# Kernel optimization log

Hardware: AMD Instinct MI355X
Metric: run time of the kernel (lower is better)

## Reference

```python
import jax, jax.numpy as jnp
import numpy as np

EPS = 1e-5

def _make_mask(rng, outdim, indim, expand_size, k=3):
    # Mirrors ExpanderConv2d mask construction (indim <= outdim branch when equal)
    m = np.zeros((outdim, indim), dtype=np.float32)
    if indim > outdim:
        for i in range(outdim):
            idx = rng.permutation(indim)[:expand_size]
            m[i, idx] = 1.0
    else:
        for i in range(indim):
            idx = rng.permutation(outdim)[:expand_size]
            m[idx, i] = 1.0
    return jnp.asarray(np.broadcast_to(m[:, :, None, None], (outdim, indim, k, k)).copy())

def _bn(x, gamma, beta, mean, var):
    # eval-mode BatchNorm2d over channel axis (NCHW)
    inv = gamma / jnp.sqrt(var + EPS)
    return x * inv[None, :, None, None] + (beta - mean * inv)[None, :, None, None]

def _conv3x3(x, w, stride=1):
    return jax.lax.conv_general_dilated(
        x, w, window_strides=(stride, stride), padding=((1, 1), (1, 1)),
        dimension_numbers=('NCHW', 'OIHW', 'NCHW'))

def setup_inputs() -> dict:
    key = jax.random.key(0)
    ks = jax.random.split(key, 4)
    C = 256
    x = jax.random.normal(ks[0], (64, C, 32, 32), dtype=jnp.float32)
    fan_out = C * 9
    std = float(np.sqrt(2.0 / fan_out))  # kaiming_normal_, mode='fan_out'
    w1 = jax.random.normal(ks[1], (C, C, 3, 3), dtype=jnp.float32) * std
    w2 = jax.random.normal(ks[2], (C, C, 3, 3), dtype=jnp.float32) * std
    rng = np.random.default_rng(0)
    mask1 = _make_mask(rng, C, C, C // 8)
    mask2 = _make_mask(rng, C, C, C // 8)
    g = jax.random.uniform(ks[3], (4 * C,), minval=0.5, maxval=1.5, dtype=jnp.float32)
    return {
        'x': x,
        'bn1_gamma': g[:C], 'bn1_beta': jnp.zeros((C,), jnp.float32),
        'bn1_mean': jnp.zeros((C,), jnp.float32), 'bn1_var': jnp.ones((C,), jnp.float32),
        'w1': w1, 'mask1': mask1,
        'bn2_gamma': g[C:2 * C], 'bn2_beta': jnp.zeros((C,), jnp.float32),
        'bn2_mean': jnp.zeros((C,), jnp.float32), 'bn2_var': jnp.ones((C,), jnp.float32),
        'w2': w2, 'mask2': mask2,
    }

def reference(x, bn1_gamma, bn1_beta, bn1_mean, bn1_var, w1, mask1,
              bn2_gamma, bn2_beta, bn2_mean, bn2_var, w2, mask2):
    out = jax.nn.relu(_bn(x, bn1_gamma, bn1_beta, bn1_mean, bn1_var))
    out = _conv3x3(out, w1 * mask1)          # masked expander conv, dropout(p=0)=identity
    out = jax.nn.relu(_bn(out, bn2_gamma, bn2_beta, bn2_mean, bn2_var))
    out = _conv3x3(out, w2 * mask2, stride=1)
    return out + x                            # identity shortcut (stride=1, in==out)
```

## Files before the change

### kernel.cpp

```cpp
#include <hip/hip_runtime.h>
#include <hip/hip_bf16.h>
#include <stdint.h>

typedef __bf16 bf16_t;
typedef __bf16 bf16x8 __attribute__((ext_vector_type(8)));
typedef __bf16 bf16x4 __attribute__((ext_vector_type(4)));
typedef float  f32x4  __attribute__((ext_vector_type(4)));

#define AS_GLOBAL __attribute__((address_space(1)))
#define AS_LDS    __attribute__((address_space(3)))

static constexpr int CCH   = 256;
static constexpr int HP    = 34;
static constexpr int PLANE = HP * HP;

__global__ void prep_params_k(const float* g1, const float* b1, const float* m1, const float* v1,
                              const float* g2, const float* b2, const float* m2, const float* v2,
                              float* prm) {
  int i = threadIdx.x;
  float i1 = g1[i] * rsqrtf(v1[i] + 1e-5f);
  prm[i]       = i1;
  prm[256 + i] = b1[i] - m1[i] * i1;
  float i2 = g2[i] * rsqrtf(v2[i] + 1e-5f);
  prm[512 + i] = i2;
  prm[768 + i] = b2[i] - m2[i] * i2;
}

__global__ __launch_bounds__(256) void prep_weights_k(const float* __restrict__ w,
                                                      const float* __restrict__ msk,
                                                      bf16_t* __restrict__ out) {
  int idx = blockIdx.x * 256 + threadIdx.x;
  const float* wp = w + (long)idx * 9;
  const float* mp = msk + (long)idx * 9;
#pragma unroll
  for (int khw = 0; khw < 9; ++khw)
    out[khw * 65536 + idx] = (bf16_t)(wp[khw] * mp[khw]);
}

__global__ __launch_bounds__(256) void zero_borders_k(bf16_t* __restrict__ t0p,
                                                      bf16_t* __restrict__ t1p) {
  const int bid = blockIdx.x;
  bf16_t* base = ((bid & 1) ? t1p : t0p) + (long)(bid >> 1) * PLANE * CCH;
  for (int i = threadIdx.x; i < 132 * 32; i += 256) {
    int pix = i >> 5, c16 = i & 31;
    int r, col;
    if (pix < 34)       { r = 0;           col = pix; }
    else if (pix < 68)  { r = 33;          col = pix - 34; }
    else if (pix < 100) { r = pix - 68 + 1; col = 0; }
    else                { r = pix - 100 + 1; col = 33; }
    *(f32x4*)&base[(r * HP + col) * CCH + c16 * 8] = f32x4{0.f, 0.f, 0.f, 0.f};
  }
}

__global__ __launch_bounds__(256) void prep_input_k(const float* __restrict__ x,
                                                    const float* __restrict__ prm,
                                                    bf16_t* __restrict__ t0p) {
  __shared__ __align__(16) bf16_t tile[64 * 256];
  const int tid = threadIdx.x;
  const int bid = blockIdx.x;
  const int n   = bid >> 4;
  const int p0  = (bid & 15) << 6;
  const int px    = tid & 63;
  const int cbase = tid >> 6;
  for (int r = 0; r < 64; ++r) {
    int ci = r * 4 + cbase;
    float v = x[((n * 256 + ci) << 10) + p0 + px];
    float y = fmaxf(v * prm[ci] + prm[256 + ci], 0.f);
    int byte = px * 512 + ((ci * 2) ^ ((px & 7) << 4));
    *(bf16_t*)((char*)tile + byte) = (bf16_t)y;
  }
  __syncthreads();
  for (int j = 0; j < 8; ++j) {
    int off  = j * 256 + tid;
    int pix  = off >> 5;
    int c16  = off & 31;
    int byte = pix * 512 + ((c16 * 16) ^ ((pix & 7) << 4));
    bf16x8 v = *(const bf16x8*)((char*)tile + byte);
    int p = p0 + pix;
    long gp = ((long)n * PLANE + ((p >> 5) + 1) * HP + (p & 31) + 1) * CCH + c16 * 8;
    *(bf16x8*)(t0p + gp) = v;
  }
}

template <int EPI>
__global__ __launch_bounds__(256, 2) void conv3x3_k(const bf16_t* __restrict__ inp,
                                                    const bf16_t* __restrict__ wts,
                                                    const float* __restrict__ prm,
                                                    const float* __restrict__ resid,
                                                    bf16_t* __restrict__ out_cl,
                                                    float* __restrict__ out_f) {
  __shared__ __align__(128) bf16_t As[2][4096];
  __shared__ __align__(128) bf16_t Bs[2][8192];

  const int tid  = threadIdx.x;
  const int lane = tid & 63;
  const int wid  = tid >> 6;
  const int wm   = wid >> 1;
  const int wn   = wid & 1;

  const int bid = blockIdx.x;
  const int w   = ((bid & 7) << 7) + (bid >> 3);
  const int co0 = (w & 1) << 7;
  const int pt  = w >> 1;
  const int n   = pt >> 3;
  const int hb  = (pt & 7) << 2;

  const int swz8 = (((lane & 3) ^ ((lane >> 2) & 3) ^ (lane >> 4)) << 3);
  const int l15  = lane & 15;

  f32x4 acc[4][4];
#pragma unroll
  for (int i = 0; i < 4; ++i)
#pragma unroll
    for (int j = 0; j < 4; ++j) acc[i][j] = f32x4{0.f, 0.f, 0.f, 0.f};

  auto stageA = [&](int ab, int c, int t) {
    const int ci0 = c << 5;
#pragma unroll
    for (int j = 0; j < 2; ++j) {
      const int ch  = wid * 2 + j;
      const int row = ch * 16 + (lane >> 2);
      const bf16_t* ga = wts + ((t * CCH + co0 + row) * CCH + ci0 + swz8);
      __builtin_amdgcn_global_load_lds((const AS_GLOBAL void*)ga,
                                       (AS_LDS void*)(&As[ab][ch * 512]), 16, 0, 0);
    }
  };

  auto stageB = [&](int bb, int c) {
    const int ci0 = c << 5;
#pragma unroll
    for (int j = 0; j < 4; ++j) {
      const int ibase = wid * 4 + j;
      int g = (ibase << 6) + lane;
      if (g > 815) g = 815;
      const int r  = g / 136;
      const int rm = g - r * 136;
      const bf16_t* gb = inp + ((n * PLANE + (hb + r) * HP + (rm >> 2)) * CCH + ci0 + ((rm & 3) << 3));
      __builtin_amdgcn_global_load_lds((const AS_GLOBAL void*)gb,
                                       (AS_LDS void*)(&Bs[bb][ibase * 512]), 16, 0, 0);
    }
  };

  stageB(0, 0);
  stageA(0, 0, 0);
  int ab = 0, bb = 0;
  for (int c = 0; c < 8; ++c) {
#pragma unroll
    for (int t = 0; t < 9; ++t) {
      __syncthreads();
      if (t < 8) stageA(ab ^ 1, c, t + 1);
      else if (c < 7) { stageB(bb ^ 1, c + 1); stageA(ab ^ 1, c + 1, 0); }
      const int kh = t / 3, kw = t - kh * 3;
      bf16x8 av[4], bv[4];
#pragma unroll
      for (int mi = 0; mi < 4; ++mi)
        av[mi] = *(const bf16x8*)&As[ab][((wm * 64 + mi * 16 + l15) << 5) + swz8];
#pragma unroll
      for (int ni = 0; ni < 4; ++ni) {
        const int p  = (wn << 6) + (ni << 4) + l15;
        const int pr = p >> 5, pc = p & 31;
        bv[ni] = *(const bf16x8*)&Bs[bb][((pr + kh) * 136 + (pc + kw) * 4 + (lane >> 4)) * 8];
      }
#pragma unroll
      for (int mi = 0; mi < 4; ++mi)
#pragma unroll
        for (int ni = 0; ni < 4; ++ni)
          acc[mi][ni] = __builtin_amdgcn_mfma_f32_16x16x32_bf16(av[mi], bv[ni], acc[mi][ni], 0, 0, 0);
      ab ^= 1;
    }
    bb ^= 1;
  }

  if (EPI == 0) {
#pragma unroll
    for (int mi = 0; mi < 4; ++mi) {
      const int co_b = co0 + wm * 64 + mi * 16 + ((lane >> 4) << 2);
      const float s0 = prm[co_b], s1 = prm[co_b + 1], s2 = prm[co_b + 2], s3 = prm[co_b + 3];
      const float t0 = prm[256 + co_b], t1 = prm[256 + co_b + 1],
                  t2 = prm[256 + co_b + 2], t3 = prm[256 + co_b + 3];
#pragma unroll
      for (int ni = 0; ni < 4; ++ni) {
        f32x4 v = acc[mi][ni];
        const int p  = (wn << 6) + (ni << 4) + l15;
        const int pr = p >> 5, pc = p & 31;
        bf16x4 pk;
        pk[0] = (bf16_t)fmaxf(v[0] * s0 + t0, 0.f);
        pk[1] = (bf16_t)fmaxf(v[1] * s1 + t1, 0.f);
        pk[2] = (bf16_t)fmaxf(v[2] * s2 + t2, 0.f);
        pk[3] = (bf16_t)fmaxf(v[3] * s3 + t3, 0.f);
        *(bf16x4*)&out_cl[(n * PLANE + (hb + pr + 1) * HP + pc + 1) * CCH + co_b] = pk;
      }
    }
  } else {
#pragma unroll
    for (int mi = 0; mi < 4; ++mi) {
      const int co_b = co0 + wm * 64 + mi * 16 + ((lane >> 4) << 2);
#pragma unroll
      for (int ni = 0; ni < 4; ++ni) {
        f32x4 v = acc[mi][ni];
        const int p  = (wn << 6) + (ni << 4) + l15;
        const int gp = ((n * CCH + co_b) << 10) + (hb << 5) + p;
        out_f[gp]        = v[0] + resid[gp];
        out_f[gp + 1024] = v[1] + resid[gp + 1024];
        out_f[gp + 2048] = v[2] + resid[gp + 2048];
        out_f[gp + 3072] = v[3] + resid[gp + 3072];
      }
    }
  }
}

extern "C" void kernel_launch(void* const* d_in, const int* in_sizes, int n_in,
                              void* d_out, int out_size, void* d_ws, size_t ws_size,
                              hipStream_t stream) {
  const float* x  = (const float*)d_in[0];
  const float* g1 = (const float*)d_in[1];
  const float* b1 = (const float*)d_in[2];
  const float* m1 = (const float*)d_in[3];
  const float* v1 = (const float*)d_in[4];
  const float* w1 = (const float*)d_in[5];
  const float* k1 = (const float*)d_in[6];
  const float* g2 = (const float*)d_in[7];
  const float* b2 = (const float*)d_in[8];
  const float* m2 = (const float*)d_in[9];
  const float* v2 = (const float*)d_in[10];
  const float* w2 = (const float*)d_in[11];
  const float* k2 = (const float*)d_in[12];

  char* ws = (char*)d_ws;
  const size_t T0P_B = (size_t)64 * PLANE * CCH * 2;
  bf16_t* t0p = (bf16_t*)ws;
  bf16_t* t1p = (bf16_t*)(ws + T0P_B);
  bf16_t* mw1 = (bf16_t*)(ws + 2 * T0P_B);
  bf16_t* mw2 = (bf16_t*)(ws + 2 * T0P_B + 1179648);
  float*  prm = (float*)(ws + 2 * T0P_B + 2 * 1179648);

  prep_params_k<<<1, 256, 0, stream>>>(g1, b1, m1, v1, g2, b2, m2, v2, prm);
  zero_borders_k<<<128, 256, 0, stream>>>(t0p, t1p);
  prep_weights_k<<<256, 256, 0, stream>>>(w1, k1, mw1);
  prep_weights_k<<<256, 256, 0, stream>>>(w2, k2, mw2);
  prep_input_k<<<1024, 256, 0, stream>>>(x, prm, t0p);

  conv3x3_k<0><<<1024, 256, 0, stream>>>(t0p, mw1, prm + 512, nullptr, t1p, nullptr);
  conv3x3_k<1><<<1024, 256, 0, stream>>>(t1p, mw2, nullptr, x, nullptr, (float*)d_out);
}
```

Before: 200.6 us.

## Deepen weight prefetch to five LDS buffers with explicit vmcnt waits

Turns the double-buffered weight (A) staging into a 5-deep ring that runs four taps ahead. It replaces __syncthreads with partial s_waitcnt vmcnt plus s_barrier, so async global-to-LDS loads stay in flight across iterations. It also rotates the B-tile channel-chunk placement to cut LDS bank conflicts on the shifted-window reads, and peels the last channel chunk into its own loop. LDS per block grows from 48KB to 72KB, which may cut occupancy below the two blocks per CU requested by launch_bounds. The hand-counted vmcnt values are fragile.

Result: no change. 203.3 us (+1.3%).

```diff
diff --git a/kernel.cpp b/kernel.cpp
--- a/kernel.cpp
+++ b/kernel.cpp
@@ -9,6 +9,7 @@
 
 #define AS_GLOBAL __attribute__((address_space(1)))
 #define AS_LDS    __attribute__((address_space(3)))
+#define VMW(N) asm volatile("s_waitcnt vmcnt(" #N ")" ::: "memory")
 
 static constexpr int CCH   = 256;
 static constexpr int HP    = 34;
@@ -89,7 +90,7 @@
                                                     const float* __restrict__ resid,
                                                     bf16_t* __restrict__ out_cl,
                                                     float* __restrict__ out_f) {
-  __shared__ __align__(128) bf16_t As[2][4096];
+  __shared__ __align__(128) bf16_t As[5][4096];
   __shared__ __align__(128) bf16_t Bs[2][8192];
 
   const int tid  = threadIdx.x;
@@ -107,6 +108,7 @@
 
   const int swz8 = (((lane & 3) ^ ((lane >> 2) & 3) ^ (lane >> 4)) << 3);
   const int l15  = lane & 15;
+  const int k4   = lane >> 4;
 
   f32x4 acc[4][4];
 #pragma unroll
@@ -114,7 +116,7 @@
 #pragma unroll
     for (int j = 0; j < 4; ++j) acc[i][j] = f32x4{0.f, 0.f, 0.f, 0.f};
 
-  auto stageA = [&](int ab, int c, int t) {
+  auto stageA = [&](int abuf, int c, int t) {
     const int ci0 = c << 5;
 #pragma unroll
     for (int j = 0; j < 2; ++j) {
@@ -122,53 +124,73 @@
       const int row = ch * 16 + (lane >> 2);
       const bf16_t* ga = wts + ((t * CCH + co0 + row) * CCH + ci0 + swz8);
       __builtin_amdgcn_global_load_lds((const AS_GLOBAL void*)ga,
-                                       (AS_LDS void*)(&As[ab][ch * 512]), 16, 0, 0);
+                                       (AS_LDS void*)(&As[abuf][ch * 512]), 16, 0, 0);
     }
   };
 
-  auto stageB = [&](int bb, int c) {
+  auto stageB = [&](int bbuf, int c) {
     const int ci0 = c << 5;
 #pragma unroll
     for (int j = 0; j < 4; ++j) {
       const int ibase = wid * 4 + j;
-      int g = (ibase << 6) + lane;
-      if (g > 815) g = 815;
-      const int r  = g / 136;
-      const int rm = g - r * 136;
-      const bf16_t* gb = inp + ((n * PLANE + (hb + r) * HP + (rm >> 2)) * CCH + ci0 + ((rm & 3) << 3));
+      int s = (ibase << 6) + lane;
+      if (s > 815) s = 815;
+      const int r     = s / 136;
+      const int rem   = s - r * 136;
+      const int cc    = rem >> 2;
+      const int k     = ((rem & 3) - (cc >> 1)) & 3;
+      const bf16_t* gb = inp + ((n * PLANE + (hb + r) * HP + cc) * CCH + ci0 + (k << 3));
       __builtin_amdgcn_global_load_lds((const AS_GLOBAL void*)gb,
-                                       (AS_LDS void*)(&Bs[bb][ibase * 512]), 16, 0, 0);
+                                       (AS_LDS void*)(&Bs[bbuf][ibase * 512]), 16, 0, 0);
     }
   };
 
+  auto compute = [&](int abuf, int bbuf, int kh, int kw) {
+    bf16x8 av[4], bv[4];
+#pragma unroll
+    for (int mi = 0; mi < 4; ++mi)
+      av[mi] = *(const bf16x8*)&As[abuf][((wm * 64 + mi * 16 + l15) << 5) + swz8];
+#pragma unroll
+    for (int ni = 0; ni < 4; ++ni) {
+      const int p    = (wn << 6) + (ni << 4) + l15;
+      const int cc   = (p & 31) + kw;
+      const int slot = ((p >> 5) + kh) * 136 + (cc << 2) + ((k4 + (cc >> 1)) & 3);
+      bv[ni] = *(const bf16x8*)&Bs[bbuf][slot << 3];
+    }
+#pragma unroll
+    for (int mi = 0; mi < 4; ++mi)
+#pragma unroll
+      for (int ni = 0; ni < 4; ++ni)
+        acc[mi][ni] = __builtin_amdgcn_mfma_f32_16x16x32_bf16(av[mi], bv[ni], acc[mi][ni], 0, 0, 0);
+  };
+
   stageB(0, 0);
-  stageA(0, 0, 0);
-  int ab = 0, bb = 0;
-  for (int c = 0; c < 8; ++c) {
+  stageA(0, 0, 0); stageA(1, 0, 1); stageA(2, 0, 2); stageA(3, 0, 3);
+
+  int ab = 0;
+  for (int c = 0; c < 7; ++c) {
 #pragma unroll
     for (int t = 0; t < 9; ++t) {
-      __syncthreads();
-      if (t < 8) stageA(ab ^ 1, c, t + 1);
-      else if (c < 7) { stageB(bb ^ 1, c + 1); stageA(ab ^ 1, c + 1, 0); }
-      const int kh = t / 3, kw = t - kh * 3;
-      bf16x8 av[4], bv[4];
-#pragma unroll
-      for (int mi = 0; mi < 4; ++mi)
-        av[mi] = *(const bf16x8*)&As[ab][((wm * 64 + mi * 16 + l15) << 5) + swz8];
-#pragma unroll
-      for (int ni = 0; ni < 4; ++ni) {
-        const int p  = (wn << 6) + (ni << 4) + l15;
-        const int pr = p >> 5, pc = p & 31;
-        bv[ni] = *(const bf16x8*)&Bs[bb][((pr + kh) * 136 + (pc + kw) * 4 + (lane >> 4)) * 8];
-      }
-#pragma unroll
-      for (int mi = 0; mi < 4; ++mi)
-#pragma unroll
-        for (int ni = 0; ni < 4; ++ni)
-          acc[mi][ni] = __builtin_amdgcn_mfma_f32_16x16x32_bf16(av[mi], bv[ni], acc[mi][ni], 0, 0, 0);
-      ab ^= 1;
-    }
-    bb ^= 1;
+      if (t >= 1 && t <= 3) { VMW(10); } else { VMW(6); }
+      __builtin_amdgcn_s_barrier();
+      if (t == 0) stageB((c + 1) & 1, c + 1);
+      int aw = ab + 4; if (aw >= 5) aw -= 5;
+      if (t < 5) stageA(aw, c, t + 4);
+      else       stageA(aw, c + 1, t - 5);
+      compute(ab, c & 1, t / 3, t % 3);
+      ++ab; if (ab == 5) ab = 0;
+    }
+  }
+#pragma unroll
+  for (int t = 0; t < 9; ++t) {
+    if      (t == 6) { VMW(4); }
+    else if (t == 7) { VMW(2); }
+    else if (t == 8) { VMW(0); }
+    else             { VMW(6); }
+    __builtin_amdgcn_s_barrier();
+    if (t < 5) { int aw = ab + 4; if (aw >= 5) aw -= 5; stageA(aw, 7, t + 4); }
+    compute(ab, 1, t / 3, t % 3);
+    ++ab; if (ab == 5) ab = 0;
   }
 
   if (EPI == 0) {
```

## Enlarge conv tile to 256x256 with 8 waves and triple-buffered weight pipeline

Applied to the files above, without the earlier changes.

Each block now computes all 256 output channels for 8 rows (256 pixels) using 512 threads, so the input halo tile is staged once per block instead of twice. Weights are triple-buffered and loaded in halves, with explicit vmcnt waits, raw barriers and setprio around the MFMA groups to overlap loads with compute. The B tile gets a rotated swizzle to reduce LDS bank conflicts. The grid shrinks to 256 blocks, which is about one block per CU on this chip and may leave little latency hiding. The larger accumulator (128 floats per lane) also adds register pressure.

Measured after the change: 193.9 us. 3.3% less time.

```diff
diff --git a/kernel.cpp b/kernel.cpp
--- a/kernel.cpp
+++ b/kernel.cpp
@@ -9,6 +9,7 @@
 
 #define AS_GLOBAL __attribute__((address_space(1)))
 #define AS_LDS    __attribute__((address_space(3)))
+#define VMW(N) asm volatile("s_waitcnt vmcnt(" #N ")" ::: "memory")
 
 static constexpr int CCH   = 256;
 static constexpr int HP    = 34;
@@ -83,98 +84,131 @@
 }
 
 template <int EPI>
-__global__ __launch_bounds__(256, 2) void conv3x3_k(const bf16_t* __restrict__ inp,
+__global__ __launch_bounds__(512, 2) void conv3x3_k(const bf16_t* __restrict__ inp,
                                                     const bf16_t* __restrict__ wts,
                                                     const float* __restrict__ prm,
                                                     const float* __restrict__ resid,
                                                     bf16_t* __restrict__ out_cl,
                                                     float* __restrict__ out_f) {
-  __shared__ __align__(128) bf16_t As[2][4096];
-  __shared__ __align__(128) bf16_t Bs[2][8192];
+  __shared__ __align__(128) bf16_t As[3][8192];
+  __shared__ __align__(128) bf16_t Bs[2][12288];
 
   const int tid  = threadIdx.x;
   const int lane = tid & 63;
   const int wid  = tid >> 6;
-  const int wm   = wid >> 1;
-  const int wn   = wid & 1;
+  const int wm   = wid >> 2;
+  const int wn   = wid & 3;
 
   const int bid = blockIdx.x;
-  const int w   = ((bid & 7) << 7) + (bid >> 3);
-  const int co0 = (w & 1) << 7;
-  const int pt  = w >> 1;
-  const int n   = pt >> 3;
-  const int hb  = (pt & 7) << 2;
+  const int n   = bid >> 2;
+  const int hb  = (bid & 3) << 3;
 
   const int swz8 = (((lane & 3) ^ ((lane >> 2) & 3) ^ (lane >> 4)) << 3);
   const int l15  = lane & 15;
-
-  f32x4 acc[4][4];
-#pragma unroll
-  for (int i = 0; i < 4; ++i)
+  const int k4   = lane >> 4;
+
+  f32x4 acc[8][4];
+#pragma unroll
+  for (int i = 0; i < 8; ++i)
 #pragma unroll
     for (int j = 0; j < 4; ++j) acc[i][j] = f32x4{0.f, 0.f, 0.f, 0.f};
 
-  auto stageA = [&](int ab, int c, int t) {
-    const int ci0 = c << 5;
-#pragma unroll
-    for (int j = 0; j < 2; ++j) {
-      const int ch  = wid * 2 + j;
-      const int row = ch * 16 + (lane >> 2);
-      const bf16_t* ga = wts + ((t * CCH + co0 + row) * CCH + ci0 + swz8);
-      __builtin_amdgcn_global_load_lds((const AS_GLOBAL void*)ga,
-                                       (AS_LDS void*)(&As[ab][ch * 512]), 16, 0, 0);
-    }
+  bf16x8 av[8], bv[4];
+
+  auto stageA_half = [&](int abuf, int c, int t, int half) {
+    const int ch  = wid * 2 + half;
+    const int row = ch * 16 + (lane >> 2);
+    const bf16_t* ga = wts + ((t * CCH + row) * CCH + (c << 5) + swz8);
+    __builtin_amdgcn_global_load_lds((const AS_GLOBAL void*)ga,
+                                     (AS_LDS void*)(&As[abuf][ch * 512]), 16, 0, 0);
   };
 
-  auto stageB = [&](int bb, int c) {
-    const int ci0 = c << 5;
-#pragma unroll
-    for (int j = 0; j < 4; ++j) {
-      const int ibase = wid * 4 + j;
-      int g = (ibase << 6) + lane;
-      if (g > 815) g = 815;
-      const int r  = g / 136;
-      const int rm = g - r * 136;
-      const bf16_t* gb = inp + ((n * PLANE + (hb + r) * HP + (rm >> 2)) * CCH + ci0 + ((rm & 3) << 3));
-      __builtin_amdgcn_global_load_lds((const AS_GLOBAL void*)gb,
-                                       (AS_LDS void*)(&Bs[bb][ibase * 512]), 16, 0, 0);
-    }
+  auto stageB = [&](int bbuf, int c, int j) {
+    const int ibase = wid * 3 + j;
+    int s = (ibase << 6) + lane;
+    if (s > 1359) s = 1359;
+    const int r   = s / 136;
+    const int rem = s - r * 136;
+    const int cc  = rem >> 2;
+    const int ks  = ((rem & 3) - (cc >> 1)) & 3;
+    const bf16_t* gb = inp + ((n * PLANE + (hb + r) * HP + cc) * CCH + (c << 5) + (ks << 3));
+    __builtin_amdgcn_global_load_lds((const AS_GLOBAL void*)gb,
+                                     (AS_LDS void*)(&Bs[bbuf][ibase * 512]), 16, 0, 0);
   };
 
-  stageB(0, 0);
-  stageA(0, 0, 0);
-  int ab = 0, bb = 0;
-  for (int c = 0; c < 8; ++c) {
-#pragma unroll
-    for (int t = 0; t < 9; ++t) {
-      __syncthreads();
-      if (t < 8) stageA(ab ^ 1, c, t + 1);
-      else if (c < 7) { stageB(bb ^ 1, c + 1); stageA(ab ^ 1, c + 1, 0); }
-      const int kh = t / 3, kw = t - kh * 3;
-      bf16x8 av[4], bv[4];
-#pragma unroll
-      for (int mi = 0; mi < 4; ++mi)
-        av[mi] = *(const bf16x8*)&As[ab][((wm * 64 + mi * 16 + l15) << 5) + swz8];
-#pragma unroll
-      for (int ni = 0; ni < 4; ++ni) {
-        const int p  = (wn << 6) + (ni << 4) + l15;
-        const int pr = p >> 5, pc = p & 31;
-        bv[ni] = *(const bf16x8*)&Bs[bb][((pr + kh) * 136 + (pc + kw) * 4 + (lane >> 4)) * 8];
-      }
-#pragma unroll
-      for (int mi = 0; mi < 4; ++mi)
-#pragma unroll
-        for (int ni = 0; ni < 4; ++ni)
-          acc[mi][ni] = __builtin_amdgcn_mfma_f32_16x16x32_bf16(av[mi], bv[ni], acc[mi][ni], 0, 0, 0);
-      ab ^= 1;
-    }
-    bb ^= 1;
-  }
+#define LDA(AB) do {                                                                \
+    _Pragma("unroll") for (int mi = 0; mi < 8; ++mi)                                \
+      av[mi] = *(const bf16x8*)&As[AB][((wm * 128 + mi * 16 + l15) << 5) + swz8];   \
+  } while (0)
+
+#define LDB(T, BB) do {                                                             \
+    constexpr int KH = (T) / 3, KW = (T) % 3;                                       \
+    _Pragma("unroll") for (int ni = 0; ni < 4; ++ni) {                              \
+      const int p_    = (wn << 6) + (ni << 4) + l15;                                \
+      const int cc_   = (p_ & 31) + KW;                                             \
+      const int slot_ = ((p_ >> 5) + KH) * 136 + (cc_ << 2) + ((k4 + (cc_ >> 1)) & 3); \
+      bv[ni] = *(const bf16x8*)&Bs[BB][slot_ << 3];                                 \
+    }                                                                               \
+  } while (0)
+
+#define MFMA8(NJ) do {                                                              \
+    _Pragma("unroll") for (int mi = 0; mi < 8; ++mi)                                \
+      acc[mi][NJ] = __builtin_amdgcn_mfma_f32_16x16x32_bf16(av[mi], bv[NJ], acc[mi][NJ], 0, 0, 0); \
+  } while (0)
+
+#define TILE(t, CL7) do {                                                           \
+    constexpr int AB  = (t) % 3;                                                    \
+    constexpr int AB2 = ((t) + 2) % 3;                                              \
+    const int bb = c & 1;                                                           \
+                                       \
+    LDA(AB); LDB(t, bb);                                                            \
+    if ((CL7) && ((t) == 1 || (t) == 3 || (t) == 5)) stageB(bb ^ 1, c + 1, ((t) - 1) / 2); \
+    if ((CL7) || (t) <= 6) {                                                        \
+      if ((t) <= 6) stageA_half(AB2, c, (t) + 2, 0);                                \
+      else          stageA_half(AB2, c + 1, (t) - 7, 0);                            \
+    }                                                                               \
+    __builtin_amdgcn_s_barrier();                                                   \
+    asm volatile("s_waitcnt lgkmcnt(0)" ::: "memory");                              \
+    __builtin_amdgcn_sched_barrier(0);                                              \
+    __builtin_amdgcn_s_setprio(1); MFMA8(0); MFMA8(1); __builtin_amdgcn_s_setprio(0); \
+    __builtin_amdgcn_s_barrier();                                                   \
+                                   \
+    if ((CL7) || (t) <= 6) {                                                        \
+      if ((t) <= 6) stageA_half(AB2, c, (t) + 2, 1);                                \
+      else          stageA_half(AB2, c + 1, (t) - 7, 1);                            \
+    }                                                                               \
+    __builtin_amdgcn_s_setprio(1); MFMA8(2); MFMA8(3); __builtin_amdgcn_s_setprio(0); \
+    if ((CL7) || (t) <= 6) {                                                        \
+      if ((CL7) && ((t) == 1 || (t) == 3 || (t) == 5)) { VMW(3); } else { VMW(2); } \
+    } else if ((t) == 7) { VMW(0); }                                                \
+    __builtin_amdgcn_s_barrier();                                                   \
+  } while (0)
+
+  stageB(0, 0, 0); stageB(0, 0, 1); stageB(0, 0, 2);
+  stageA_half(0, 0, 0, 0); stageA_half(0, 0, 0, 1);
+  stageA_half(1, 0, 1, 0); stageA_half(1, 0, 1, 1);
+  VMW(2);
+  __builtin_amdgcn_s_barrier();
+
+  for (int c = 0; c < 7; ++c) {
+    TILE(0, 1); TILE(1, 1); TILE(2, 1); TILE(3, 1); TILE(4, 1);
+    TILE(5, 1); TILE(6, 1); TILE(7, 1); TILE(8, 1);
+  }
+  {
+    const int c = 7;
+    TILE(0, 0); TILE(1, 0); TILE(2, 0); TILE(3, 0); TILE(4, 0);
+    TILE(5, 0); TILE(6, 0); TILE(7, 0); TILE(8, 0);
+  }
+
+#undef TILE
+#undef LDA
+#undef LDB
+#undef MFMA8
 
   if (EPI == 0) {
 #pragma unroll
-    for (int mi = 0; mi < 4; ++mi) {
-      const int co_b = co0 + wm * 64 + mi * 16 + ((lane >> 4) << 2);
+    for (int mi = 0; mi < 8; ++mi) {
+      const int co_b = wm * 128 + mi * 16 + ((lane >> 4) << 2);
       const float s0 = prm[co_b], s1 = prm[co_b + 1], s2 = prm[co_b + 2], s3 = prm[co_b + 3];
       const float t0 = prm[256 + co_b], t1 = prm[256 + co_b + 1],
                   t2 = prm[256 + co_b + 2], t3 = prm[256 + co_b + 3];
@@ -193,8 +227,8 @@
     }
   } else {
 #pragma unroll
-    for (int mi = 0; mi < 4; ++mi) {
-      const int co_b = co0 + wm * 64 + mi * 16 + ((lane >> 4) << 2);
+    for (int mi = 0; mi < 8; ++mi) {
+      const int co_b = wm * 128 + mi * 16 + ((lane >> 4) << 2);
 #pragma unroll
       for (int ni = 0; ni < 4; ++ni) {
         f32x4 v = acc[mi][ni];
@@ -240,6 +274,6 @@
   prep_weights_k<<<256, 256, 0, stream>>>(w2, k2, mw2);
   prep_input_k<<<1024, 256, 0, stream>>>(x, prm, t0p);
 
-  conv3x3_k<0><<<1024, 256, 0, stream>>>(t0p, mw1, prm + 512, nullptr, t1p, nullptr);
-  conv3x3_k<1><<<1024, 256, 0, stream>>>(t1p, mw2, nullptr, x, nullptr, (float*)d_out);
-}
+  conv3x3_k<0><<<256, 512, 0, stream>>>(t0p, mw1, prm + 512, nullptr, t1p, nullptr);
+  conv3x3_k<1><<<256, 512, 0, stream>>>(t1p, mw2, nullptr, x, nullptr, (float*)d_out);
+}
```

## Enlarge conv tile to 256x256 with triple-buffered weights and register prefetch

Applied to the files above, without the earlier changes.

Each block now computes all 256 output channels over 8 image rows, so each wave holds an 8x8 grid of MFMA accumulators and reuses loaded fragments more. Weights are staged through three LDS buffers and input through two, with B staging spread across taps and explicit vmcnt/lgkmcnt waits. Fragments for the next tap are prefetched into alternate register sets while the current MFMAs run. This cuts global and LDS traffic per FLOP, at the cost of occupancy (one block per CU, 256 blocks) and heavy register pressure.

Measured after the change: 379.9 us. +89.3%, slower.

```diff
diff --git a/kernel.cpp b/kernel.cpp
--- a/kernel.cpp
+++ b/kernel.cpp
@@ -9,6 +9,7 @@
 
 #define AS_GLOBAL __attribute__((address_space(1)))
 #define AS_LDS    __attribute__((address_space(3)))
+#define VMW(N) asm volatile("s_waitcnt vmcnt(" #N ")" ::: "memory")
 
 static constexpr int CCH   = 256;
 static constexpr int HP    = 34;
@@ -83,14 +84,14 @@
 }
 
 template <int EPI>
-__global__ __launch_bounds__(256, 2) void conv3x3_k(const bf16_t* __restrict__ inp,
+__global__ __launch_bounds__(256, 1) void conv3x3_k(const bf16_t* __restrict__ inp,
                                                     const bf16_t* __restrict__ wts,
                                                     const float* __restrict__ prm,
                                                     const float* __restrict__ resid,
                                                     bf16_t* __restrict__ out_cl,
                                                     float* __restrict__ out_f) {
-  __shared__ __align__(128) bf16_t As[2][4096];
-  __shared__ __align__(128) bf16_t Bs[2][8192];
+  __shared__ __align__(128) bf16_t As[3][8192];
+  __shared__ __align__(128) bf16_t Bs[2][12288];
 
   const int tid  = threadIdx.x;
   const int lane = tid & 63;
@@ -99,89 +100,127 @@
   const int wn   = wid & 1;
 
   const int bid = blockIdx.x;
-  const int w   = ((bid & 7) << 7) + (bid >> 3);
-  const int co0 = (w & 1) << 7;
-  const int pt  = w >> 1;
-  const int n   = pt >> 3;
-  const int hb  = (pt & 7) << 2;
+  const int n   = bid >> 2;
+  const int hb  = (bid & 3) << 3;
 
   const int swz8 = (((lane & 3) ^ ((lane >> 2) & 3) ^ (lane >> 4)) << 3);
   const int l15  = lane & 15;
-
-  f32x4 acc[4][4];
-#pragma unroll
-  for (int i = 0; i < 4; ++i)
-#pragma unroll
-    for (int j = 0; j < 4; ++j) acc[i][j] = f32x4{0.f, 0.f, 0.f, 0.f};
-
-  auto stageA = [&](int ab, int c, int t) {
-    const int ci0 = c << 5;
-#pragma unroll
-    for (int j = 0; j < 2; ++j) {
-      const int ch  = wid * 2 + j;
-      const int row = ch * 16 + (lane >> 2);
-      const bf16_t* ga = wts + ((t * CCH + co0 + row) * CCH + ci0 + swz8);
+  const int k4   = lane >> 4;
+
+  const int rowq  = tid >> 2;
+  const int aslot = (tid & 3) ^ ((tid >> 2) & 3) ^ ((tid >> 4) & 3);
+  int bofs[6];
+#pragma unroll
+  for (int j = 0; j < 6; ++j) {
+    int s = j * 256 + tid; if (s > 1359) s = 1359;
+    int r = s / 136; int rem = s - r * 136; int cc = rem >> 2;
+    int ks = ((rem & 3) - (cc >> 1)) & 3;
+    bofs[j] = (n * PLANE + (hb + r) * HP + cc) * CCH + (ks << 3);
+  }
+
+  f32x4 acc[8][8];
+#pragma unroll
+  for (int i = 0; i < 8; ++i)
+#pragma unroll
+    for (int j = 0; j < 8; ++j) acc[i][j] = f32x4{0.f, 0.f, 0.f, 0.f};
+
+  bf16x8 avA[8], bvA[8], avB[8], bvB[8];
+
+  auto stageA = [&](int abuf, int cw, int tw) {
+#pragma unroll
+    for (int j = 0; j < 4; ++j) {
+      const bf16_t* ga = wts + ((tw * CCH + j * 64 + rowq) * CCH + (cw << 5) + (aslot << 3));
       __builtin_amdgcn_global_load_lds((const AS_GLOBAL void*)ga,
-                                       (AS_LDS void*)(&As[ab][ch * 512]), 16, 0, 0);
+                                       (AS_LDS void*)(&As[abuf][(j * 256 + tid) * 8]), 16, 0, 0);
     }
   };
 
-  auto stageB = [&](int bb, int c) {
-    const int ci0 = c << 5;
-#pragma unroll
-    for (int j = 0; j < 4; ++j) {
-      const int ibase = wid * 4 + j;
-      int g = (ibase << 6) + lane;
-      if (g > 815) g = 815;
-      const int r  = g / 136;
-      const int rm = g - r * 136;
-      const bf16_t* gb = inp + ((n * PLANE + (hb + r) * HP + (rm >> 2)) * CCH + ci0 + ((rm & 3) << 3));
-      __builtin_amdgcn_global_load_lds((const AS_GLOBAL void*)gb,
-                                       (AS_LDS void*)(&Bs[bb][ibase * 512]), 16, 0, 0);
-    }
-  };
-
-  stageB(0, 0);
+#define STB(J, BBUF, CN) do {                                                        \
+    const bf16_t* gb_ = inp + bofs[J] + ((CN) << 5);                                 \
+    __builtin_amdgcn_global_load_lds((const AS_GLOBAL void*)gb_,                     \
+        (AS_LDS void*)(&Bs[BBUF][((J) * 256 + tid) * 8]), 16, 0, 0);                 \
+  } while (0)
+
+#define PREF(AV, BV, AB, BB, KH, KW) do {                                            \
+    _Pragma("unroll") for (int mi = 0; mi < 8; ++mi)                                 \
+      AV[mi] = *(const bf16x8*)&As[AB][((wm * 128 + mi * 16 + l15) << 5) + swz8];    \
+    _Pragma("unroll") for (int ni = 0; ni < 8; ++ni) {                               \
+      const int p_    = (wn << 7) + (ni << 4) + l15;                                 \
+      const int cc_   = (p_ & 31) + (KW);                                            \
+      const int slot_ = ((p_ >> 5) + (KH)) * 136 + (cc_ << 2) + ((k4 + (cc_ >> 1)) & 3); \
+      BV[ni] = *(const bf16x8*)&Bs[BB][slot_ << 3];                                  \
+    }                                                                                \
+  } while (0)
+
+#define MFMA64(AV, BV) do {                                                          \
+    _Pragma("unroll") for (int mi = 0; mi < 8; ++mi)                                 \
+    _Pragma("unroll") for (int ni = 0; ni < 8; ++ni)                                 \
+      acc[mi][ni] = __builtin_amdgcn_mfma_f32_16x16x32_bf16(AV[mi], BV[ni], acc[mi][ni], 0, 0, 0); \
+  } while (0)
+
+#define TILE(TAP, PAR, LASTC) do {                                                   \
+    __builtin_amdgcn_s_barrier();                                                    \
+    if (!(LASTC) && (TAP) >= 1 && (TAP) <= 6) { STB((TAP) - 1, (PAR) ^ 1, c + 1); }  \
+    if (!((LASTC) && (TAP) >= 7)) {                                                  \
+      stageA(((TAP) + 2) % 3, ((TAP) <= 6) ? c : c + 1, ((TAP) + 2) % 9);            \
+    }                                                                                \
+    if (LASTC) { if ((TAP) <= 6) { VMW(4); } else { VMW(0); } }                      \
+    else if ((TAP) >= 1 && (TAP) <= 6) { VMW(5); }                                   \
+    else { VMW(4); }                                                                 \
+    if (!((LASTC) && (TAP) == 8)) {                                                  \
+      constexpr int T1  = ((TAP) + 1) % 9;                                           \
+      constexpr int AB1 = ((TAP) + 1) % 3;                                           \
+      constexpr int BB1 = ((TAP) < 8) ? (PAR) : ((PAR) ^ 1);                         \
+      if (((PAR) + (TAP)) & 1) { PREF(avA, bvA, AB1, BB1, T1 / 3, T1 % 3); }         \
+      else                     { PREF(avB, bvB, AB1, BB1, T1 / 3, T1 % 3); }         \
+      asm volatile("s_waitcnt lgkmcnt(15)" ::: "memory");                            \
+    } else {                                                                         \
+      asm volatile("s_waitcnt lgkmcnt(0)" ::: "memory");                             \
+    }                                                                                \
+    __builtin_amdgcn_sched_barrier(0);                                               \
+    if (((PAR) + (TAP)) & 1) { MFMA64(avB, bvB); } else { MFMA64(avA, bvA); }        \
+  } while (0)
+
+#define CH(PAR) do {                                                                 \
+    TILE(0, PAR, 0); TILE(1, PAR, 0); TILE(2, PAR, 0); TILE(3, PAR, 0);              \
+    TILE(4, PAR, 0); TILE(5, PAR, 0); TILE(6, PAR, 0); TILE(7, PAR, 0);              \
+    TILE(8, PAR, 0);                                                                 \
+  } while (0)
+
+  STB(0, 0, 0); STB(1, 0, 0); STB(2, 0, 0); STB(3, 0, 0); STB(4, 0, 0); STB(5, 0, 0);
   stageA(0, 0, 0);
-  int ab = 0, bb = 0;
-  for (int c = 0; c < 8; ++c) {
-#pragma unroll
-    for (int t = 0; t < 9; ++t) {
-      __syncthreads();
-      if (t < 8) stageA(ab ^ 1, c, t + 1);
-      else if (c < 7) { stageB(bb ^ 1, c + 1); stageA(ab ^ 1, c + 1, 0); }
-      const int kh = t / 3, kw = t - kh * 3;
-      bf16x8 av[4], bv[4];
-#pragma unroll
-      for (int mi = 0; mi < 4; ++mi)
-        av[mi] = *(const bf16x8*)&As[ab][((wm * 64 + mi * 16 + l15) << 5) + swz8];
-#pragma unroll
-      for (int ni = 0; ni < 4; ++ni) {
-        const int p  = (wn << 6) + (ni << 4) + l15;
-        const int pr = p >> 5, pc = p & 31;
-        bv[ni] = *(const bf16x8*)&Bs[bb][((pr + kh) * 136 + (pc + kw) * 4 + (lane >> 4)) * 8];
-      }
-#pragma unroll
-      for (int mi = 0; mi < 4; ++mi)
-#pragma unroll
-        for (int ni = 0; ni < 4; ++ni)
-          acc[mi][ni] = __builtin_amdgcn_mfma_f32_16x16x32_bf16(av[mi], bv[ni], acc[mi][ni], 0, 0, 0);
-      ab ^= 1;
-    }
-    bb ^= 1;
-  }
+  stageA(1, 0, 1);
+  VMW(4);
+  __builtin_amdgcn_s_barrier();
+  PREF(avA, bvA, 0, 0, 0, 0);
+
+  int c = 0;
+#pragma unroll 1
+  for (int it = 0; it < 3; ++it) {
+    CH(0); ++c;
+    CH(1); ++c;
+  }
+  CH(0); ++c;
+  TILE(0, 1, 1); TILE(1, 1, 1); TILE(2, 1, 1); TILE(3, 1, 1); TILE(4, 1, 1);
+  TILE(5, 1, 1); TILE(6, 1, 1); TILE(7, 1, 1); TILE(8, 1, 1);
+
+#undef TILE
+#undef CH
+#undef PREF
+#undef MFMA64
+#undef STB
 
   if (EPI == 0) {
 #pragma unroll
-    for (int mi = 0; mi < 4; ++mi) {
-      const int co_b = co0 + wm * 64 + mi * 16 + ((lane >> 4) << 2);
+    for (int mi = 0; mi < 8; ++mi) {
+      const int co_b = wm * 128 + mi * 16 + ((lane >> 4) << 2);
       const float s0 = prm[co_b], s1 = prm[co_b + 1], s2 = prm[co_b + 2], s3 = prm[co_b + 3];
       const float t0 = prm[256 + co_b], t1 = prm[256 + co_b + 1],
                   t2 = prm[256 + co_b + 2], t3 = prm[256 + co_b + 3];
 #pragma unroll
-      for (int ni = 0; ni < 4; ++ni) {
+      for (int ni = 0; ni < 8; ++ni) {
         f32x4 v = acc[mi][ni];
-        const int p  = (wn << 6) + (ni << 4) + l15;
+        const int p  = (wn << 7) + (ni << 4) + l15;
         const int pr = p >> 5, pc = p & 31;
         bf16x4 pk;
         pk[0] = (bf16_t)fmaxf(v[0] * s0 + t0, 0.f);
@@ -193,12 +232,12 @@
     }
   } else {
 #pragma unroll
-    for (int mi = 0; mi < 4; ++mi) {
-      const int co_b = co0 + wm * 64 + mi * 16 + ((lane >> 4) << 2);
-#pragma unroll
-      for (int ni = 0; ni < 4; ++ni) {
+    for (int mi = 0; mi < 8; ++mi) {
+      const int co_b = wm * 128 + mi * 16 + ((lane >> 4) << 2);
+#pragma unroll
+      for (int ni = 0; ni < 8; ++ni) {
         f32x4 v = acc[mi][ni];
-        const int p  = (wn << 6) + (ni << 4) + l15;
+        const int p  = (wn << 7) + (ni << 4) + l15;
         const int gp = ((n * CCH + co_b) << 10) + (hb << 5) + p;
         out_f[gp]        = v[0] + resid[gp];
         out_f[gp + 1024] = v[1] + resid[gp + 1024];
@@ -240,6 +279,6 @@
   prep_weights_k<<<256, 256, 0, stream>>>(w2, k2, mw2);
   prep_input_k<<<1024, 256, 0, stream>>>(x, prm, t0p);
 
-  conv3x3_k<0><<<1024, 256, 0, stream>>>(t0p, mw1, prm + 512, nullptr, t1p, nullptr);
-  conv3x3_k<1><<<1024, 256, 0, stream>>>(t1p, mw2, nullptr, x, nullptr, (float*)d_out);
-}
+  conv3x3_k<0><<<256, 256, 0, stream>>>(t0p, mw1, prm + 512, nullptr, t1p, nullptr);
+  conv3x3_k<1><<<256, 256, 0, stream>>>(t1p, mw2, nullptr, x, nullptr, (float*)d_out);
+}
```
